# Kernel tuning notes

Hardware: AMD Instinct MI355X
Metric: run time of the kernel (lower is better)

Reference implementation:

```python
import jax, jax.numpy as jnp
import numpy as np

N = 32768   # nodes
E = 524288  # edges (avg degree 16)
F = 32      # num_features
H = 512     # hidden_channels
C = 10      # num_classes
G = 64      # graphs in batch


def setup_inputs() -> dict:
    key = jax.random.key(0)
    ks = jax.random.split(key, 16)
    s = 0.05  # weight init scale
    f32 = jnp.float32
    return {
        "x": jax.random.normal(ks[0], (N, F), f32),
        "edge_index": jax.random.randint(ks[1], (2, E), 0, N),
        "batch_index": jnp.sort(jax.random.randint(ks[2], (N,), 0, G)),
        # initial_conv: F -> H  (PyG GraphConv: lin_root on x, lin_rel on aggregated neighbors)
        "w_root0": jax.random.normal(ks[3], (F, H), f32) * s,
        "w_rel0": jax.random.normal(ks[4], (F, H), f32) * s,
        "b0": jnp.zeros((H,), f32),
        # conv1..conv4 stacked: H -> H
        "w_root": jax.random.normal(ks[5], (4, H, H), f32) * s,
        "w_rel": jax.random.normal(ks[6], (4, H, H), f32) * s,
        "b": jnp.zeros((4, H), f32),
        # MLP tail
        "lin1_w": jax.random.normal(ks[7], (2 * H, H), f32) * s,
        "lin1_b": jnp.zeros((H,), f32),
        "lin2_w": jax.random.normal(ks[8], (H, H), f32) * s,
        "lin2_b": jnp.zeros((H,), f32),
        "lin3_w": jax.random.normal(ks[9], (H, C), f32) * s,
        "lin3_b": jnp.zeros((C,), f32),
    }


def _graph_conv(h, src, dst, w_root, w_rel, bias):
    # out_i = h_i @ W_root + (sum_{j->i} h_j) @ W_rel + b   (PyG GraphConv, aggr='add')
    agg = jax.ops.segment_sum(h[src], dst, num_segments=N)
    return h @ w_root + agg @ w_rel + bias


def reference(x, edge_index, batch_index,
              w_root0, w_rel0, b0, w_root, w_rel, b,
              lin1_w, lin1_b, lin2_w, lin2_b, lin3_w, lin3_b):
    src, dst = edge_index[0], edge_index[1]
    h = jnp.tanh(_graph_conv(x, src, dst, w_root0, w_rel0, b0))
    for i in range(4):  # fixed small layer loop
        h = jnp.tanh(_graph_conv(h, src, dst, w_root[i], w_rel[i], b[i]))
    # global max + mean pool over graphs
    gmax = jax.ops.segment_max(h, batch_index, num_segments=G)
    gsum = jax.ops.segment_sum(h, batch_index, num_segments=G)
    cnt = jax.ops.segment_sum(jnp.ones((N,), h.dtype), batch_index, num_segments=G)
    gmean = gsum / jnp.maximum(cnt, 1.0)[:, None]
    g = jnp.concatenate([gmax, gmean], axis=1)  # [G, 2H]
    # dropout is identity at inference (training=False)
    g = jnp.tanh(g @ lin1_w + lin1_b)
    g = jnp.tanh(g @ lin2_w + lin2_b)
    logits = g @ lin3_w + lin3_b
    return jax.nn.log_softmax(logits, axis=1)
```

## Files before the change

### kernel.cpp

```cpp
#include <hip/hip_runtime.h>
#include <hip/hip_bf16.h>
#include <math.h>

#define NN 32768
#define EE 524288
#define FF 32
#define HH 512
#define GG 64
#define CC 10

typedef __attribute__((ext_vector_type(8))) short short8;
typedef __attribute__((ext_vector_type(4))) float floatx4;
typedef __attribute__((ext_vector_type(4))) unsigned int uintx4;

__device__ __forceinline__ float bf16_to_f32(unsigned short u) {
    union { unsigned int u; float f; } v;
    v.u = ((unsigned int)u) << 16;
    return v.f;
}
__device__ __forceinline__ unsigned short f32_to_bf16(float f) {
    union { float f; unsigned int u; } v;
    v.f = f;
    unsigned int u = v.u;
    u += 0x7FFFu + ((u >> 16) & 1u);
    return (unsigned short)(u >> 16);
}
__device__ __forceinline__ float fast_tanh(float x) {
    float e = __expf(2.0f * x);
    return 1.0f - 2.0f * __builtin_amdgcn_rcpf(e + 1.0f);
}

__global__ void prep_all_kernel(const float* __restrict__ wr0, const float* __restrict__ wl0,
                                unsigned short* __restrict__ WT0,
                                const float* __restrict__ wroot, const float* __restrict__ wrel,
                                unsigned short* __restrict__ WTs,
                                const float* __restrict__ x, unsigned short* __restrict__ X0) {
    const int b = blockIdx.x;
    if (b < 128) {
        int t = b * 256 + threadIdx.x;
        int n = t >> 6, k = t & 63;
        float v = (k < 32) ? wr0[k * 512 + n] : wl0[(k - 32) * 512 + n];
        WT0[t] = f32_to_bf16(v);
    } else if (b < 8320) {
        int t = (b - 128) * 256 + threadIdx.x;
        int l = t >> 19;
        int r = t & 524287;
        int n = r >> 10, k = r & 1023;
        float v = (k < 512) ? wroot[(size_t)l * 262144 + k * 512 + n]
                            : wrel[(size_t)l * 262144 + (k - 512) * 512 + n];
        WTs[t] = f32_to_bf16(v);
    } else {
        int t = (b - 8320) * 256 + threadIdx.x;
        int i = t >> 5, c = t & 31;
        X0[(size_t)i * 64 + c] = f32_to_bf16(x[t]);
    }
}

__global__ void zero_i32(int* __restrict__ p, int n) {
    int i = blockIdx.x * blockDim.x + threadIdx.x;
    if (i < n) p[i] = 0;
}
__global__ void hist_kernel(const int* __restrict__ dst, int* __restrict__ counts) {
    int e = blockIdx.x * blockDim.x + threadIdx.x;
    if (e < EE) atomicAdd(&counts[dst[e]], 1);
}
__global__ __launch_bounds__(1024) void scan_kernel(const int* __restrict__ counts,
                                                    int* __restrict__ rowStart,
                                                    int* __restrict__ cursor) {
    __shared__ int part[1024];
    const int t = threadIdx.x;
    const int base = t * 32;
    int local[32];
    const int4* cp = (const int4*)(counts + base);
    int s = 0;
#pragma unroll
    for (int ii = 0; ii < 8; ++ii) {
        int4 v = cp[ii];
        local[ii * 4 + 0] = v.x; local[ii * 4 + 1] = v.y;
        local[ii * 4 + 2] = v.z; local[ii * 4 + 3] = v.w;
        s += v.x + v.y + v.z + v.w;
    }
    part[t] = s;
    __syncthreads();
    for (int off = 1; off < 1024; off <<= 1) {
        int v = (t >= off) ? part[t - off] : 0;
        __syncthreads();
        part[t] += v;
        __syncthreads();
    }
    int run = part[t] - s;
#pragma unroll
    for (int i = 0; i < 32; ++i) {
        rowStart[base + i] = run;
        cursor[base + i] = run;
        run += local[i];
    }
    if (t == 1023) rowStart[NN] = run;
}
__global__ void scatter_kernel(const int* __restrict__ src, const int* __restrict__ dst,
                               int* __restrict__ cursor, int* __restrict__ ssrc) {
    int e = blockIdx.x * blockDim.x + threadIdx.x;
    if (e < EE) {
        int p = atomicAdd(&cursor[dst[e]], 1);
        ssrc[p] = src[e];
    }
}
__global__ __launch_bounds__(256) void deg_hist_kernel(const int* __restrict__ counts,
                                                       int* __restrict__ degHist) {
    __shared__ int lh[256];
    lh[threadIdx.x] = 0;
    __syncthreads();
    int i = blockIdx.x * 256 + threadIdx.x;
    int d = counts[i]; if (d > 255) d = 255;
    atomicAdd(&lh[255 - d], 1);
    __syncthreads();
    int v = lh[threadIdx.x];
    if (v) atomicAdd(&degHist[threadIdx.x], v);
}
__global__ __launch_bounds__(256) void deg_scan_kernel(const int* __restrict__ degHist,
                                                       int* __restrict__ degCursor) {
    __shared__ int sh[256];
    const int t = threadIdx.x;
    int own = degHist[t];
    sh[t] = own;
    __syncthreads();
    for (int off = 1; off < 256; off <<= 1) {
        int v = (t >= off) ? sh[t - off] : 0;
        __syncthreads();
        sh[t] += v;
        __syncthreads();
    }
    degCursor[t] = sh[t] - own;
}
__global__ __launch_bounds__(256) void deg_scatter_kernel(const int* __restrict__ counts,
                                                          int* __restrict__ degCursor,
                                                          int* __restrict__ perm,
                                                          int* __restrict__ pDeg) {
    __shared__ int lh[256];
    __shared__ int base[256];
    lh[threadIdx.x] = 0;
    __syncthreads();
    int i = blockIdx.x * 256 + threadIdx.x;
    int dtrue = counts[i];
    int d = dtrue > 255 ? 255 : dtrue;
    int bin = 255 - d;
    int lr = atomicAdd(&lh[bin], 1);
    __syncthreads();
    int c = lh[threadIdx.x];
    if (c) base[threadIdx.x] = atomicAdd(&degCursor[threadIdx.x], c);
    __syncthreads();
    int p = base[bin] + lr;
    perm[p] = i;
    pDeg[p] = dtrue;
}
__global__ __launch_bounds__(256) void edge_copy_kernel(const int* __restrict__ rowStart,
                                                        const int* __restrict__ perm,
                                                        const int* __restrict__ pRowStart,
                                                        const int* __restrict__ ssrc,
                                                        int* __restrict__ pssrc) {
    const int wv = threadIdx.x >> 6, lane = threadIdx.x & 63;
    const int sub = lane >> 4, l16 = lane & 15;
    const int p = blockIdx.x * 16 + wv * 4 + sub;
    const int node = perm[p];
    const int s = rowStart[node], e = rowStart[node + 1];
    const int ns = pRowStart[p];
    for (int j = s + l16; j < e; j += 16) pssrc[ns + (j - s)] = ssrc[j];
}

__device__ __forceinline__ void acc8(float* a, uint4 d) {
    a[0] += bf16_to_f32((unsigned short)(d.x & 0xFFFFu));
    a[1] += bf16_to_f32((unsigned short)(d.x >> 16));
    a[2] += bf16_to_f32((unsigned short)(d.y & 0xFFFFu));
    a[3] += bf16_to_f32((unsigned short)(d.y >> 16));
    a[4] += bf16_to_f32((unsigned short)(d.z & 0xFFFFu));
    a[5] += bf16_to_f32((unsigned short)(d.z >> 16));
    a[6] += bf16_to_f32((unsigned short)(d.w & 0xFFFFu));
    a[7] += bf16_to_f32((unsigned short)(d.w >> 16));
}
__device__ __forceinline__ void acc8v(float* a, uintx4 d) {
    a[0] += bf16_to_f32((unsigned short)(d[0] & 0xFFFFu));
    a[1] += bf16_to_f32((unsigned short)(d[0] >> 16));
    a[2] += bf16_to_f32((unsigned short)(d[1] & 0xFFFFu));
    a[3] += bf16_to_f32((unsigned short)(d[1] >> 16));
    a[4] += bf16_to_f32((unsigned short)(d[2] & 0xFFFFu));
    a[5] += bf16_to_f32((unsigned short)(d[2] >> 16));
    a[6] += bf16_to_f32((unsigned short)(d[3] & 0xFFFFu));
    a[7] += bf16_to_f32((unsigned short)(d[3] >> 16));
}

__global__ __launch_bounds__(256) void agg_kernel(const unsigned short* __restrict__ Xh, int ldh,
                                                  int cols, unsigned short* __restrict__ Xagg,
                                                  int ldagg, const int* __restrict__ rowStart,
                                                  const int* __restrict__ ssrc) {
    const int node = blockIdx.x * 4 + (threadIdx.x >> 6);
    const int lane = threadIdx.x & 63;
    const int chunks = cols >> 3;
    if (node >= NN || lane >= chunks) return;
    const int s = rowStart[node];
    const int e = rowStart[node + 1];
    float a[8] = {0.f, 0.f, 0.f, 0.f, 0.f, 0.f, 0.f, 0.f};
    const unsigned short* base = Xh + lane * 8;
    int i = s;
    for (; i + 4 <= e; i += 4) {
        int j0 = ssrc[i], j1 = ssrc[i + 1], j2 = ssrc[i + 2], j3 = ssrc[i + 3];
        uint4 d0 = *(const uint4*)(base + (size_t)j0 * ldh);
        uint4 d1 = *(const uint4*)(base + (size_t)j1 * ldh);
        uint4 d2 = *(const uint4*)(base + (size_t)j2 * ldh);
        uint4 d3 = *(const uint4*)(base + (size_t)j3 * ldh);
        acc8(a, d0); acc8(a, d1); acc8(a, d2); acc8(a, d3);
    }
    for (; i < e; ++i) {
        int j = ssrc[i];
        uint4 d = *(const uint4*)(base + (size_t)j * ldh);
        acc8(a, d);
    }
    unsigned short* out = Xagg + (size_t)node * ldagg + lane * 8;
#pragma unroll
    for (int c = 0; c < 8; ++c) out[c] = f32_to_bf16(a[c]);
}

#define GLOAD(dreg, voff) \
    asm volatile("buffer_load_dwordx4 %0, %1, %2, 0 offen" \
                 : "=v"(dreg) : "v"(voff), "s"(srsrc))

__global__ __launch_bounds__(256, 3) void agg_slice_kernel(const unsigned short* __restrict__ Xh,
                                                           unsigned short* __restrict__ Xagg,
                                                           const int* __restrict__ pRowStart,
                                                           const int* __restrict__ pssrc,
                                                           const int* __restrict__ perm) {
    const int slice = blockIdx.x & 7;
    const int pair = blockIdx.x >> 3;
    const int wv = threadIdx.x >> 6;
    const int lane = threadIdx.x & 63;
    const int ln = lane >> 3;
    const int lc = lane & 7;
    const int colOff = slice * 64 + lc * 8;
    const unsigned short* base = Xh + colOff;
    uintx4 srsrc;
    {
        union { const unsigned short* p; unsigned int u[2]; } ba;
        ba.p = Xh + slice * 64;
        srsrc[0] = ba.u[0];
        srsrc[1] = ba.u[1] & 0xFFFFu;
        srsrc[2] = 0xFFFFFFFFu;
        srsrc[3] = 0x00020000u;
    }
    const unsigned int lcoff = (unsigned int)(lc << 4);
#pragma unroll
    for (int half = 0; half < 2; ++half) {
        const int nb = half ? (1023 - pair) : pair;
        const int p = nb * 32 + wv * 8 + ln;
        const int node = perm[p];
        const int s = pRowStart[p];
        const int e = pRowStart[p + 1];
        float a[8] = {0.f, 0.f, 0.f, 0.f, 0.f, 0.f, 0.f, 0.f};
        int i = s;
        for (; i + 16 <= e; i += 16) {
            unsigned int vo[16];
#pragma unroll
            for (int u = 0; u < 16; ++u)
                vo[u] = (((unsigned int)pssrc[i + u]) << 11) | lcoff;
            uintx4 d0, d1, d2, d3, d4, d5, d6, d7, d8, d9, d10, d11, d12, d13, d14, d15;
            __builtin_amdgcn_sched_barrier(0);
            GLOAD(d0, vo[0]);   GLOAD(d1, vo[1]);   GLOAD(d2, vo[2]);   GLOAD(d3, vo[3]);
            GLOAD(d4, vo[4]);   GLOAD(d5, vo[5]);   GLOAD(d6, vo[6]);   GLOAD(d7, vo[7]);
            GLOAD(d8, vo[8]);   GLOAD(d9, vo[9]);   GLOAD(d10, vo[10]); GLOAD(d11, vo[11]);
            GLOAD(d12, vo[12]); GLOAD(d13, vo[13]); GLOAD(d14, vo[14]); GLOAD(d15, vo[15]);
            asm volatile("s_waitcnt vmcnt(8)" ::: "memory");
            __builtin_amdgcn_sched_barrier(0);
            acc8v(a, d0); acc8v(a, d1); acc8v(a, d2); acc8v(a, d3);
            acc8v(a, d4); acc8v(a, d5); acc8v(a, d6); acc8v(a, d7);
            asm volatile("s_waitcnt vmcnt(0)" ::: "memory");
            __builtin_amdgcn_sched_barrier(0);
            acc8v(a, d8);  acc8v(a, d9);  acc8v(a, d10); acc8v(a, d11);
            acc8v(a, d12); acc8v(a, d13); acc8v(a, d14); acc8v(a, d15);
        }
        if (e - i >= 8) {
            unsigned int vo[8];
#pragma unroll
            for (int u = 0; u < 8; ++u)
                vo[u] = (((unsigned int)pssrc[i + u]) << 11) | lcoff;
            uintx4 d0, d1, d2, d3, d4, d5, d6, d7;
            __builtin_amdgcn_sched_barrier(0);
            GLOAD(d0, vo[0]); GLOAD(d1, vo[1]); GLOAD(d2, vo[2]); GLOAD(d3, vo[3]);
            GLOAD(d4, vo[4]); GLOAD(d5, vo[5]); GLOAD(d6, vo[6]); GLOAD(d7, vo[7]);
            asm volatile("s_waitcnt vmcnt(4)" ::: "memory");
            __builtin_amdgcn_sched_barrier(0);
            acc8v(a, d0); acc8v(a, d1); acc8v(a, d2); acc8v(a, d3);
            asm volatile("s_waitcnt vmcnt(0)" ::: "memory");
            __builtin_amdgcn_sched_barrier(0);
            acc8v(a, d4); acc8v(a, d5); acc8v(a, d6); acc8v(a, d7);
            i += 8;
        }
        for (; i + 4 <= e; i += 4) {
            int j0 = pssrc[i], j1 = pssrc[i + 1], j2 = pssrc[i + 2], j3 = pssrc[i + 3];
            uint4 e0 = *(const uint4*)(base + (size_t)j0 * 1024);
            uint4 e1 = *(const uint4*)(base + (size_t)j1 * 1024);
            uint4 e2 = *(const uint4*)(base + (size_t)j2 * 1024);
            uint4 e3 = *(const uint4*)(base + (size_t)j3 * 1024);
            acc8(a, e0); acc8(a, e1); acc8(a, e2); acc8(a, e3);
        }
        for (; i < e; ++i) {
            int j = pssrc[i];
            uint4 d = *(const uint4*)(base + (size_t)j * 1024);
            acc8(a, d);
        }
        unsigned short* out = Xagg + (size_t)node * 1024 + colOff;
#pragma unroll
        for (int c = 0; c < 8; ++c) out[c] = f32_to_bf16(a[c]);
    }
}

__global__ __launch_bounds__(256, 4) void gemm_bias_tanh(const unsigned short* __restrict__ Xin,
                                                         int ldin, int K,
                                                         const unsigned short* __restrict__ WT,
                                                         const float* __restrict__ bias,
                                                         unsigned short* __restrict__ Xout,
                                                         int ldout) {
    __shared__ __align__(16) unsigned short As[128 * 64];
    __shared__ __align__(16) unsigned short Bs[128 * 64];
    const int tid = threadIdx.x;
    const int lane = tid & 63;
    const int wave = tid >> 6;
    const int wm = wave >> 1, wn = wave & 1;
    const int bm = blockIdx.x, bn = blockIdx.y;

    floatx4 acc[4][4] = {};

    const int lrow = lane >> 3;
    const int schunk = (lane & 7) ^ (lrow & 7);
    const unsigned short* Abase = Xin + (size_t)(bm * 128) * ldin;
    const unsigned short* Bbase = WT + (size_t)(bn * 128) * K;
    const int m = lane & 15;
    const int quad = lane >> 4;

    for (int k0 = 0; k0 < K; k0 += 64) {
        __syncthreads();
#pragma unroll
        for (int q = 0; q < 4; ++q) {
            const int rr = q * 32 + wave * 8;
            const int row = rr + lrow;
            const unsigned short* sa = Abase + (size_t)row * ldin + (k0 + schunk * 8);
            const unsigned short* sb = Bbase + (size_t)row * K + (k0 + schunk * 8);
            __builtin_amdgcn_global_load_lds(
                (const __attribute__((address_space(1))) void*)sa,
                (__attribute__((address_space(3))) void*)(&As[rr * 64]), 16, 0, 0);
            __builtin_amdgcn_global_load_lds(
                (const __attribute__((address_space(1))) void*)sb,
                (__attribute__((address_space(3))) void*)(&Bs[rr * 64]), 16, 0, 0);
        }
        __syncthreads();
#pragma unroll
        for (int half = 0; half < 2; ++half) {
            short8 af[4], bfr[4];
#pragma unroll
            for (int t = 0; t < 4; ++t) {
                const int row = wm * 64 + t * 16 + m;
                const int chunk = (half * 4 + quad) ^ (row & 7);
                af[t] = *(const short8*)&As[row * 64 + chunk * 8];
            }
#pragma unroll
            for (int t = 0; t < 4; ++t) {
                const int row = wn * 64 + t * 16 + m;
                const int chunk = (half * 4 + quad) ^ (row & 7);
                bfr[t] = *(const short8*)&Bs[row * 64 + chunk * 8];
            }
#pragma unroll
            for (int mt = 0; mt < 4; ++mt)
#pragma unroll
                for (int nt = 0; nt < 4; ++nt)
                    acc[mt][nt] = __builtin_amdgcn_mfma_f32_16x16x32_bf16(af[mt], bfr[nt],
                                                                          acc[mt][nt], 0, 0, 0);
        }
    }

    const int row0 = bm * 128 + wm * 64;
    const int col0 = bn * 128 + wn * 64;
#pragma unroll
    for (int mt = 0; mt < 4; ++mt) {
#pragma unroll
        for (int nt = 0; nt < 4; ++nt) {
            const int col = col0 + nt * 16 + m;
            const float bv = bias[col];
#pragma unroll
            for (int r = 0; r < 4; ++r) {
                const int row = row0 + mt * 16 + quad * 4 + r;
                float v = fast_tanh(acc[mt][nt][r] + bv);
                Xout[(size_t)row * ldout + col] = f32_to_bf16(v);
            }
        }
    }
}

__global__ __launch_bounds__(256) void pool_partial(const unsigned short* __restrict__ h,
                                                    const int* __restrict__ batch,
                                                    float* __restrict__ part) {
    const int gi = blockIdx.x, rs = blockIdx.y, t = threadIdx.x;
    int lo = 0, hi = NN;
    while (lo < hi) { int mid = (lo + hi) >> 1; if (batch[mid] < gi) lo = mid + 1; else hi = mid; }
    const int start = lo;
    hi = NN;
    while (lo < hi) { int mid = (lo + hi) >> 1; if (batch[mid] < gi + 1) lo = mid + 1; else hi = mid; }
    const int end = lo;
    const int len = end - start;
    const int q = (len + 7) >> 3;
    int r0 = start + rs * q;
    int r1 = r0 + q; if (r1 > end) r1 = end; if (r0 > end) r0 = end;
    float mx0 = -INFINITY, mx1 = -INFINITY, s0 = 0.f, s1 = 0.f;
    int i = r0;
    for (; i + 2 <= r1; i += 2) {
        unsigned int d0 = *(const unsigned int*)(h + (size_t)i * 1024 + t * 2);
        unsigned int d1 = *(const unsigned int*)(h + (size_t)(i + 1) * 1024 + t * 2);
        float v0 = bf16_to_f32((unsigned short)(d0 & 0xFFFFu));
        float v1 = bf16_to_f32((unsigned short)(d0 >> 16));
        float w0 = bf16_to_f32((unsigned short)(d1 & 0xFFFFu));
        float w1 = bf16_to_f32((unsigned short)(d1 >> 16));
        mx0 = fmaxf(mx0, fmaxf(v0, w0)); mx1 = fmaxf(mx1, fmaxf(v1, w1));
        s0 += v0 + w0; s1 += v1 + w1;
    }
    for (; i < r1; ++i) {
        unsigned int d0 = *(const unsigned int*)(h + (size_t)i * 1024 + t * 2);
        float v0 = bf16_to_f32((unsigned short)(d0 & 0xFFFFu));
        float v1 = bf16_to_f32((unsigned short)(d0 >> 16));
        mx0 = fmaxf(mx0, v0); mx1 = fmaxf(mx1, v1);
        s0 += v0; s1 += v1;
    }
    float* p = part + ((size_t)gi * 8 + rs) * 1024;
    p[t * 2] = mx0; p[t * 2 + 1] = mx1;
    p[512 + t * 2] = s0; p[512 + t * 2 + 1] = s1;
}

__global__ __launch_bounds__(256) void pool_combine(const float* __restrict__ part,
                                                    const int* __restrict__ batch,
                                                    float* __restrict__ gT) {
    const int gi = blockIdx.x, t = threadIdx.x;
    int lo = 0, hi = NN;
    while (lo < hi) { int mid = (lo + hi) >> 1; if (batch[mid] < gi) lo = mid + 1; else hi = mid; }
    const int start = lo;
    hi = NN;
    while (lo < hi) { int mid = (lo + hi) >> 1; if (batch[mid] < gi + 1) lo = mid + 1; else hi = mid; }
    int cnt = lo - start; if (cnt < 1) cnt = 1;
    const float inv = 1.0f / (float)cnt;
    float mx0 = -INFINITY, mx1 = -INFINITY, s0 = 0.f, s1 = 0.f;
#pragma unroll
    for (int rs = 0; rs < 8; ++rs) {
        const float* p = part + ((size_t)gi * 8 + rs) * 1024;
        mx0 = fmaxf(mx0, p[t * 2]); mx1 = fmaxf(mx1, p[t * 2 + 1]);
        s0 += p[512 + t * 2]; s1 += p[512 + t * 2 + 1];
    }
    gT[(size_t)(2 * t) * 64 + gi]        = mx0;
    gT[(size_t)(2 * t + 1) * 64 + gi]    = mx1;
    gT[(size_t)(512 + 2 * t) * 64 + gi]  = s0 * inv;
    gT[(size_t)(512 + 2 * t + 1) * 64 + gi] = s1 * inv;
}

__global__ __launch_bounds__(256) void mlp_splitk(const float* __restrict__ ginT,
                                                  const float* __restrict__ W,
                                                  int Ndim,
                                                  float* __restrict__ partial) {
    __shared__ float gsT[64][68];
    __shared__ float Ws[64][68];
    const int t = threadIdx.x;
    const int wv = t >> 6, l = t & 63;
    const int nb = blockIdx.x, kb = blockIdx.y;
    const int n0 = nb * 64;
    const int gr = t >> 2;
    const int c4 = (t & 3) * 16;
    float acc[16] = {};
#pragma unroll
    for (int sub = 0; sub < 2; ++sub) {
        const int k0 = kb * 128 + sub * 64;
        __syncthreads();
        {
            const float4* gsrc = (const float4*)(ginT + (size_t)(k0 + gr) * 64 + c4);
            float4* gd = (float4*)&gsT[gr][c4];
            gd[0] = gsrc[0]; gd[1] = gsrc[1]; gd[2] = gsrc[2]; gd[3] = gsrc[3];
            const float4* wsrc = (const float4*)(W + (size_t)(k0 + gr) * Ndim + n0 + c4);
            float4* wd = (float4*)&Ws[gr][c4];
            wd[0] = wsrc[0]; wd[1] = wsrc[1]; wd[2] = wsrc[2]; wd[3] = wsrc[3];
        }
        __syncthreads();
#pragma unroll 4
        for (int kk = 0; kk < 64; ++kk) {
            const float wval = Ws[kk][l];
            const float4* gv = (const float4*)&gsT[kk][wv * 16];
            float4 g0 = gv[0], g1 = gv[1], g2 = gv[2], g3 = gv[3];
            acc[0]  = fmaf(g0.x, wval, acc[0]);  acc[1]  = fmaf(g0.y, wval, acc[1]);
            acc[2]  = fmaf(g0.z, wval, acc[2]);  acc[3]  = fmaf(g0.w, wval, acc[3]);
            acc[4]  = fmaf(g1.x, wval, acc[4]);  acc[5]  = fmaf(g1.y, wval, acc[5]);
            acc[6]  = fmaf(g1.z, wval, acc[6]);  acc[7]  = fmaf(g1.w, wval, acc[7]);
            acc[8]  = fmaf(g2.x, wval, acc[8]);  acc[9]  = fmaf(g2.y, wval, acc[9]);
            acc[10] = fmaf(g2.z, wval, acc[10]); acc[11] = fmaf(g2.w, wval, acc[11]);
            acc[12] = fmaf(g3.x, wval, acc[12]); acc[13] = fmaf(g3.y, wval, acc[13]);
            acc[14] = fmaf(g3.z, wval, acc[14]); acc[15] = fmaf(g3.w, wval, acc[15]);
        }
    }
    float* p = partial + ((size_t)kb * 64) * Ndim;
#pragma unroll
    for (int g = 0; g < 16; ++g)
        p[(size_t)(wv * 16 + g) * Ndim + n0 + l] = acc[g];
}

__global__ __launch_bounds__(256) void mlp_combine(const float* __restrict__ partial, int nparts,
                                                   const float* __restrict__ bias, int Ndim,
                                                   float* __restrict__ outN,
                                                   float* __restrict__ outT) {
    const int idx = blockIdx.x * 256 + threadIdx.x;
    if (idx >= 64 * Ndim) return;
    const int g = idx / Ndim, n = idx - g * Ndim;
    float s = bias[n];
    for (int kb = 0; kb < nparts; ++kb)
        s += partial[((size_t)kb * 64 + g) * Ndim + n];
    const float v = fast_tanh(s);
    if (outN) outN[(size_t)g * Ndim + n] = v;
    if (outT) outT[(size_t)n * 64 + g] = v;
}

__global__ __launch_bounds__(64) void head_kernel(const float* __restrict__ g2,
                                                  const float* __restrict__ W,
                                                  const float* __restrict__ b,
                                                  float* __restrict__ out) {
    const int gi = blockIdx.x, t = threadIdx.x;
    const float4* gp = (const float4*)(g2 + (size_t)gi * HH + t * 8);
    float4 ga = gp[0], gb = gp[1];
    float gv[8] = {ga.x, ga.y, ga.z, ga.w, gb.x, gb.y, gb.z, gb.w};
    float logits[CC];
#pragma unroll
    for (int c = 0; c < CC; ++c) {
        float p = 0.f;
#pragma unroll
        for (int j = 0; j < 8; ++j)
            p = fmaf(gv[j], W[(t * 8 + j) * CC + c], p);
#pragma unroll
        for (int off = 32; off > 0; off >>= 1)
            p += __shfl_xor(p, off, 64);
        logits[c] = p + b[c];
    }
    if (t == 0) {
        float mx = logits[0];
#pragma unroll
        for (int c = 1; c < CC; ++c) mx = fmaxf(mx, logits[c]);
        float s = 0.f;
#pragma unroll
        for (int c = 0; c < CC; ++c) s += expf(logits[c] - mx);
        float lse = mx + logf(s);
#pragma unroll
        for (int c = 0; c < CC; ++c) out[(size_t)gi * CC + c] = logits[c] - lse;
    }
}

extern "C" void kernel_launch(void* const* d_in, const int* in_sizes, int n_in,
                              void* d_out, int out_size, void* d_ws, size_t ws_size,
                              hipStream_t stream) {
    const float* x       = (const float*)d_in[0];
    const int*   ei      = (const int*)d_in[1];
    const int*   batch   = (const int*)d_in[2];
    const float* w_root0 = (const float*)d_in[3];
    const float* w_rel0  = (const float*)d_in[4];
    const float* b0      = (const float*)d_in[5];
    const float* w_root  = (const float*)d_in[6];
    const float* w_rel   = (const float*)d_in[7];
    const float* bvec    = (const float*)d_in[8];
    const float* lin1_w  = (const float*)d_in[9];
    const float* lin1_b  = (const float*)d_in[10];
    const float* lin2_w  = (const float*)d_in[11];
    const float* lin2_b  = (const float*)d_in[12];
    const float* lin3_w  = (const float*)d_in[13];
    const float* lin3_b  = (const float*)d_in[14];
    float* out = (float*)d_out;

    char* w = (char*)d_ws;
    size_t off = 0;
    auto alloc = [&](size_t bytes) -> char* {
        char* p = w + off;
        off += (bytes + 255) & ~(size_t)255;
        return p;
    };
    unsigned short* Xa  = (unsigned short*)alloc((size_t)NN * 1024 * 2);
    unsigned short* Xb  = (unsigned short*)alloc((size_t)NN * 1024 * 2);
    unsigned short* X0  = (unsigned short*)alloc((size_t)NN * 64 * 2);
    unsigned short* WT0 = (unsigned short*)alloc(512 * 64 * 2);
    unsigned short* WTs = (unsigned short*)alloc((size_t)4 * 512 * 1024 * 2);
    int* counts   = (int*)alloc((size_t)NN * 4);
    int* degHist  = (int*)alloc(256 * 4);
    int* degCursor= (int*)alloc(256 * 4);
    int* rowStart = (int*)alloc((size_t)(NN + 1) * 4);
    int* cursor   = (int*)alloc((size_t)NN * 4);
    int* ssrc     = (int*)alloc((size_t)EE * 4);
    int* perm     = (int*)alloc((size_t)NN * 4);
    int* pDeg     = (int*)alloc((size_t)NN * 4);
    int* pRowStart= (int*)alloc((size_t)(NN + 1) * 4);
    int* pCursor  = (int*)alloc((size_t)NN * 4);
    int* pssrc    = (int*)alloc((size_t)EE * 4);
    float* gbufT  = (float*)alloc((size_t)1024 * 64 * 4);
    float* g1T    = (float*)alloc((size_t)512 * 64 * 4);
    float* g2buf  = (float*)alloc((size_t)GG * 512 * 4);
    float* mlpPart = (float*)alloc((size_t)8 * 64 * 512 * 4);
    float* part   = (float*)X0;

    const int* esrc = ei;
    const int* edst = ei + EE;

    prep_all_kernel<<<12416, 256, 0, stream>>>(w_root0, w_rel0, WT0, w_root, w_rel, WTs, x, X0);
    zero_i32<<<130, 256, 0, stream>>>(counts, NN + 256);
    hist_kernel<<<2048, 256, 0, stream>>>(edst, counts);
    scan_kernel<<<1, 1024, 0, stream>>>(counts, rowStart, cursor);
    scatter_kernel<<<2048, 256, 0, stream>>>(esrc, edst, cursor, ssrc);
    deg_hist_kernel<<<128, 256, 0, stream>>>(counts, degHist);
    deg_scan_kernel<<<1, 256, 0, stream>>>(degHist, degCursor);
    deg_scatter_kernel<<<128, 256, 0, stream>>>(counts, degCursor, perm, pDeg);
    scan_kernel<<<1, 1024, 0, stream>>>(pDeg, pRowStart, pCursor);
    edge_copy_kernel<<<2048, 256, 0, stream>>>(rowStart, perm, pRowStart, ssrc, pssrc);

    agg_kernel<<<8192, 256, 0, stream>>>(X0, 64, 32, X0 + 32, 64, rowStart, ssrc);
    gemm_bias_tanh<<<dim3(256, 4), 256, 0, stream>>>(X0, 64, 64, WT0, b0, Xa, 1024);

    agg_slice_kernel<<<4096, 256, 0, stream>>>(Xa, Xa + 512, pRowStart, pssrc, perm);
    gemm_bias_tanh<<<dim3(256, 4), 256, 0, stream>>>(Xa, 1024, 1024, WTs + 0 * 524288, bvec + 0, Xb, 1024);
    agg_slice_kernel<<<4096, 256, 0, stream>>>(Xb, Xb + 512, pRowStart, pssrc, perm);
    gemm_bias_tanh<<<dim3(256, 4), 256, 0, stream>>>(Xb, 1024, 1024, WTs + 1 * 524288, bvec + 512, Xa, 1024);
    agg_slice_kernel<<<4096, 256, 0, stream>>>(Xa, Xa + 512, pRowStart, pssrc, perm);
    gemm_bias_tanh<<<dim3(256, 4), 256, 0, stream>>>(Xa, 1024, 1024, WTs + 2 * 524288, bvec + 1024, Xb, 1024);
    agg_slice_kernel<<<4096, 256, 0, stream>>>(Xb, Xb + 512, pRowStart, pssrc, perm);
    gemm_bias_tanh<<<dim3(256, 4), 256, 0, stream>>>(Xb, 1024, 1024, WTs + 3 * 524288, bvec + 1536, Xa, 1024);

    pool_partial<<<dim3(GG, 8), 256, 0, stream>>>(Xa, batch, part);
    pool_combine<<<GG, 256, 0, stream>>>(part, batch, gbufT);
    mlp_splitk<<<dim3(8, 8), 256, 0, stream>>>(gbufT, lin1_w, 512, mlpPart);
    mlp_combine<<<128, 256, 0, stream>>>(mlpPart, 8, lin1_b, 512, nullptr, g1T);
    mlp_splitk<<<dim3(8, 4), 256, 0, stream>>>(g1T, lin2_w, 512, mlpPart);
    mlp_combine<<<128, 256, 0, stream>>>(mlpPart, 4, lin2_b, 512, g2buf, nullptr);
    head_kernel<<<GG, 64, 0, stream>>>(g2buf, lin3_w, lin3_b, out);
}
```

Measured before the change: 643.1 us.

## Add 256x256-tile double-buffered GEMM with direct-to-LDS loads for hidden layers

Replaces the 128x128-tile GEMM for the four hidden-layer convolutions with a 256x256-tile, 512-thread kernel. It stages tiles through global_load_lds into swizzled LDS, double-buffers them and interleaves the prefetch with MFMA phases, and reorders block IDs for L2 locality. The aggregation kernel also gets nontemporal index loads and a single packed 16-byte nontemporal store instead of eight scalar stores. The larger tile cuts global/LDS traffic per FLOP but uses 128KB of LDS and many accumulator registers, which limits occupancy.

```diff
diff --git a/kernel.cpp b/kernel.cpp
--- a/kernel.cpp
+++ b/kernel.cpp
@@ -259,7 +259,7 @@
             unsigned int vo[16];
 #pragma unroll
             for (int u = 0; u < 16; ++u)
-                vo[u] = (((unsigned int)pssrc[i + u]) << 11) | lcoff;
+                vo[u] = (((unsigned int)__builtin_nontemporal_load(&pssrc[i + u])) << 11) | lcoff;
             uintx4 d0, d1, d2, d3, d4, d5, d6, d7, d8, d9, d10, d11, d12, d13, d14, d15;
             __builtin_amdgcn_sched_barrier(0);
             GLOAD(d0, vo[0]);   GLOAD(d1, vo[1]);   GLOAD(d2, vo[2]);   GLOAD(d3, vo[3]);
@@ -279,7 +279,7 @@
             unsigned int vo[8];
 #pragma unroll
             for (int u = 0; u < 8; ++u)
-                vo[u] = (((unsigned int)pssrc[i + u]) << 11) | lcoff;
+                vo[u] = (((unsigned int)__builtin_nontemporal_load(&pssrc[i + u])) << 11) | lcoff;
             uintx4 d0, d1, d2, d3, d4, d5, d6, d7;
             __builtin_amdgcn_sched_barrier(0);
             GLOAD(d0, vo[0]); GLOAD(d1, vo[1]); GLOAD(d2, vo[2]); GLOAD(d3, vo[3]);
@@ -306,8 +306,12 @@
             acc8(a, d);
         }
         unsigned short* out = Xagg + (size_t)node * 1024 + colOff;
-#pragma unroll
-        for (int c = 0; c < 8; ++c) out[c] = f32_to_bf16(a[c]);
+        uintx4 ov;
+        ov[0] = (unsigned int)f32_to_bf16(a[0]) | ((unsigned int)f32_to_bf16(a[1]) << 16);
+        ov[1] = (unsigned int)f32_to_bf16(a[2]) | ((unsigned int)f32_to_bf16(a[3]) << 16);
+        ov[2] = (unsigned int)f32_to_bf16(a[4]) | ((unsigned int)f32_to_bf16(a[5]) << 16);
+        ov[3] = (unsigned int)f32_to_bf16(a[6]) | ((unsigned int)f32_to_bf16(a[7]) << 16);
+        __builtin_nontemporal_store(ov, (uintx4*)out);
     }
 }
 
@@ -386,6 +390,179 @@
             for (int r = 0; r < 4; ++r) {
                 const int row = row0 + mt * 16 + quad * 4 + r;
                 float v = fast_tanh(acc[mt][nt][r] + bv);
+                Xout[(size_t)row * ldout + col] = f32_to_bf16(v);
+            }
+        }
+    }
+}
+
+__device__ __forceinline__ void stage_half(const unsigned short* __restrict__ gsrc0,
+                                           int ldg, unsigned short* ldsHalf,
+                                           int w, int lane) {
+#pragma unroll
+    for (int q = 0; q < 2; ++q) {
+        const int rb = q * 64 + w * 8;
+        const unsigned short* src = gsrc0 + (size_t)(rb + (lane >> 3)) * ldg
+                                    + ((lane & 7) ^ (lane >> 3)) * 8;
+        __builtin_amdgcn_global_load_lds(
+            (const __attribute__((address_space(1))) void*)src,
+            (__attribute__((address_space(3))) void*)(ldsHalf + rb * 64), 16, 0, 0);
+    }
+}
+__device__ __forceinline__ void stage_q(const unsigned short* __restrict__ gsrc0,
+                                        int ldg, unsigned short* ldsQ,
+                                        int w, int lane) {
+    const unsigned short* src = gsrc0 + (size_t)(w * 8 + (lane >> 3)) * ldg
+                                + ((lane & 7) ^ (lane >> 3)) * 8;
+    __builtin_amdgcn_global_load_lds(
+        (const __attribute__((address_space(1))) void*)src,
+        (__attribute__((address_space(3))) void*)(ldsQ + (w * 8) * 64), 16, 0, 0);
+}
+
+__global__ __launch_bounds__(512, 2) void gemm256_bias_tanh(
+    const unsigned short* __restrict__ Xin, int ldin, int K,
+    const unsigned short* __restrict__ WT, const float* __restrict__ bias,
+    unsigned short* __restrict__ Xout, int ldout) {
+    __shared__ __align__(16) unsigned short As[2][256 * 64];
+    __shared__ __align__(16) unsigned short Bs[2][256 * 64];
+    const int tid = threadIdx.x;
+    const int lane = tid & 63;
+    const int w = tid >> 6;
+    const int wm = w >> 2, wn = w & 3;
+    const int m = lane & 15, quad = lane >> 4;
+    const int id = (int)blockIdx.x;
+    const int bm = (id & 7) * 16 + (id >> 4);
+    const int bn = (id >> 3) & 1;
+    const int NT = K >> 6;
+
+    const unsigned short* Abase = Xin + (size_t)(bm * 256) * ldin;
+    const unsigned short* Bbase = WT + (size_t)(bn * 256) * K;
+
+    floatx4 acc[8][4] = {};
+
+#define STG_AH(buf, h, kt_) stage_half(Abase + (size_t)((h) * 128) * ldin + (kt_) * 64, ldin, \
+                                       &As[buf][(h) * 128 * 64], w, lane)
+#define STG_BH(buf, h, kt_) stage_half(Bbase + (size_t)((h) * 128) * K + (kt_) * 64, K, \
+                                       &Bs[buf][(h) * 128 * 64], w, lane)
+#define STG_AQ(buf, qr, kt_) stage_q(Abase + (size_t)((qr) * 64) * ldin + (kt_) * 64, ldin, \
+                                     &As[buf][(qr) * 64 * 64], w, lane)
+
+    STG_BH(0, 0, 0); STG_BH(0, 1, 0); STG_AH(0, 0, 0); STG_AH(0, 1, 0);
+    STG_BH(1, 0, 1); STG_BH(1, 1, 1); STG_AH(1, 0, 1); STG_AH(1, 1, 1);
+    asm volatile("s_waitcnt vmcnt(8)" ::: "memory");
+    __builtin_amdgcn_s_barrier();
+
+    for (int kt = 0; kt < NT; ++kt) {
+        const int cur = kt & 1;
+        const unsigned short* Ac = &As[cur][0];
+        const unsigned short* Bc = &Bs[cur][0];
+        const bool pf = (kt + 2 < NT);
+        short8 afr[8], bfr[8];
+
+#pragma unroll
+        for (int nf = 0; nf < 4; ++nf)
+#pragma unroll
+            for (int ks = 0; ks < 2; ++ks) {
+                const int col = wn * 64 + nf * 16 + m;
+                const int chunk = (ks * 4 + quad) ^ (col & 7);
+                bfr[nf * 2 + ks] = *(const short8*)&Bc[col * 64 + chunk * 8];
+            }
+#pragma unroll
+        for (int t = 0; t < 4; ++t)
+#pragma unroll
+            for (int ks = 0; ks < 2; ++ks) {
+                const int row = wm * 128 + t * 16 + m;
+                const int chunk = (ks * 4 + quad) ^ (row & 7);
+                afr[t * 2 + ks] = *(const short8*)&Ac[row * 64 + chunk * 8];
+            }
+        __builtin_amdgcn_s_barrier();
+        __builtin_amdgcn_s_setprio(1);
+#pragma unroll
+        for (int t = 0; t < 4; ++t)
+#pragma unroll
+            for (int u = 0; u < 2; ++u)
+#pragma unroll
+                for (int ks = 0; ks < 2; ++ks)
+                    acc[t][u] = __builtin_amdgcn_mfma_f32_16x16x32_bf16(
+                        afr[t * 2 + ks], bfr[u * 2 + ks], acc[t][u], 0, 0, 0);
+        __builtin_amdgcn_s_setprio(0);
+        __builtin_amdgcn_s_barrier();
+
+        if (pf) { STG_AQ(cur, 0, kt + 2); STG_AQ(cur, 2, kt + 2); }
+        __builtin_amdgcn_s_barrier();
+        __builtin_amdgcn_s_setprio(1);
+#pragma unroll
+        for (int t = 0; t < 4; ++t)
+#pragma unroll
+            for (int u = 2; u < 4; ++u)
+#pragma unroll
+                for (int ks = 0; ks < 2; ++ks)
+                    acc[t][u] = __builtin_amdgcn_mfma_f32_16x16x32_bf16(
+                        afr[t * 2 + ks], bfr[u * 2 + ks], acc[t][u], 0, 0, 0);
+        __builtin_amdgcn_s_setprio(0);
+        __builtin_amdgcn_s_barrier();
+
+#pragma unroll
+        for (int t = 0; t < 4; ++t)
+#pragma unroll
+            for (int ks = 0; ks < 2; ++ks) {
+                const int row = wm * 128 + (4 + t) * 16 + m;
+                const int chunk = (ks * 4 + quad) ^ (row & 7);
+                afr[t * 2 + ks] = *(const short8*)&Ac[row * 64 + chunk * 8];
+            }
+        __builtin_amdgcn_sched_barrier(0);
+        if (pf) STG_BH(cur, 0, kt + 2);
+        __builtin_amdgcn_s_barrier();
+        __builtin_amdgcn_s_setprio(1);
+#pragma unroll
+        for (int t = 0; t < 4; ++t)
+#pragma unroll
+            for (int u = 0; u < 2; ++u)
+#pragma unroll
+                for (int ks = 0; ks < 2; ++ks)
+                    acc[4 + t][u] = __builtin_amdgcn_mfma_f32_16x16x32_bf16(
+                        afr[t * 2 + ks], bfr[u * 2 + ks], acc[4 + t][u], 0, 0, 0);
+        __builtin_amdgcn_s_setprio(0);
+        __builtin_amdgcn_s_barrier();
+
+        if (pf) {
+            STG_BH(cur, 1, kt + 2);
+            STG_AQ(cur, 1, kt + 2); STG_AQ(cur, 3, kt + 2);
+        }
+        __builtin_amdgcn_s_barrier();
+        __builtin_amdgcn_s_setprio(1);
+#pragma unroll
+        for (int t = 0; t < 4; ++t)
+#pragma unroll
+            for (int u = 2; u < 4; ++u)
+#pragma unroll
+                for (int ks = 0; ks < 2; ++ks)
+                    acc[4 + t][u] = __builtin_amdgcn_mfma_f32_16x16x32_bf16(
+                        afr[t * 2 + ks], bfr[u * 2 + ks], acc[4 + t][u], 0, 0, 0);
+        __builtin_amdgcn_s_setprio(0);
+        if (kt <= NT - 3) {
+            asm volatile("s_waitcnt vmcnt(8)" ::: "memory");
+        } else {
+            asm volatile("s_waitcnt vmcnt(0)" ::: "memory");
+        }
+        __builtin_amdgcn_s_barrier();
+    }
+#undef STG_AH
+#undef STG_BH
+#undef STG_AQ
+
+    const int row0 = bm * 256 + wm * 128;
+    const int col0 = bn * 256 + wn * 64;
+#pragma unroll
+    for (int mf = 0; mf < 8; ++mf) {
+#pragma unroll
+        for (int nf = 0; nf < 4; ++nf) {
+            const int col = col0 + nf * 16 + m;
+            const float bv = bias[col];
+#pragma unroll
+            for (int r = 0; r < 4; ++r) {
+                const int row = row0 + mf * 16 + quad * 4 + r;
+                float v = fast_tanh(acc[mf][nf][r] + bv);
                 Xout[(size_t)row * ldout + col] = f32_to_bf16(v);
             }
         }
@@ -616,13 +793,13 @@
     gemm_bias_tanh<<<dim3(256, 4), 256, 0, stream>>>(X0, 64, 64, WT0, b0, Xa, 1024);
 
     agg_slice_kernel<<<4096, 256, 0, stream>>>(Xa, Xa + 512, pRowStart, pssrc, perm);
-    gemm_bias_tanh<<<dim3(256, 4), 256, 0, stream>>>(Xa, 1024, 1024, WTs + 0 * 524288, bvec + 0, Xb, 1024);
+    gemm256_bias_tanh<<<256, 512, 0, stream>>>(Xa, 1024, 1024, WTs + 0 * 524288, bvec + 0, Xb, 1024);
     agg_slice_kernel<<<4096, 256, 0, stream>>>(Xb, Xb + 512, pRowStart, pssrc, perm);
-    gemm_bias_tanh<<<dim3(256, 4), 256, 0, stream>>>(Xb, 1024, 1024, WTs + 1 * 524288, bvec + 512, Xa, 1024);
+    gemm256_bias_tanh<<<256, 512, 0, stream>>>(Xb, 1024, 1024, WTs + 1 * 524288, bvec + 512, Xa, 1024);
     agg_slice_kernel<<<4096, 256, 0, stream>>>(Xa, Xa + 512, pRowStart, pssrc, perm);
-    gemm_bias_tanh<<<dim3(256, 4), 256, 0, stream>>>(Xa, 1024, 1024, WTs + 2 * 524288, bvec + 1024, Xb, 1024);
+    gemm256_bias_tanh<<<256, 512, 0, stream>>>(Xa, 1024, 1024, WTs + 2 * 524288, bvec + 1024, Xb, 1024);
     agg_slice_kernel<<<4096, 256, 0, stream>>>(Xb, Xb + 512, pRowStart, pssrc, perm);
-    gemm_bias_tanh<<<dim3(256, 4), 256, 0, stream>>>(Xb, 1024, 1024, WTs + 3 * 524288, bvec + 1536, Xa, 1024);
+    gemm256_bias_tanh<<<256, 512, 0, stream>>>(Xb, 1024, 1024, WTs + 3 * 524288, bvec + 1536, Xa, 1024);
 
     pool_partial<<<dim3(GG, 8), 256, 0, stream>>>(Xa, batch, part);
     pool_combine<<<GG, 256, 0, stream>>>(part, batch, gbufT);
```

Result: slower. 666.8 us (+3.7%).
